# Kernel optimization log

Hardware: AMD Instinct MI355X
Metric: run time of the kernel (lower is better)

## Reference

```python
import jax, jax.numpy as jnp
import numpy as np

B, S, HID = 2, 2048, 3584
H, KV, D = 16, 8, 256
RQ, RK, RV = 6, 2, 2
GRP = H // KV
EPS = 1e-6
SOFTCAP = 50.0
SCALE = 256.0 ** -0.5  # query_pre_attn_scalar ** -0.5
NEG = -2.3819763e38


def _rmsnorm(x, w):
    # Gemma RMSNorm: fp32 normalize, scale by (1 + weight)
    xf = x.astype(jnp.float32)
    n = xf * jax.lax.rsqrt(jnp.mean(xf * xf, axis=-1, keepdims=True) + EPS)
    return (n * (1.0 + w)).astype(x.dtype)


def _rope_factor(x, freqs_cis):
    # x: [B,S,R,D]; freqs_cis: [S, D/2, 2] = (cos, sin)
    h = D // 2
    cos = freqs_cis[None, :, None, :, 0]  # [1,S,1,D/2]
    sin = freqs_cis[None, :, None, :, 1]
    x1, x2 = x[..., :h], x[..., h:]
    return jnp.concatenate([x1 * cos - x2 * sin, x2 * cos + x1 * sin], axis=-1)


def setup_inputs() -> dict:
    key = jax.random.key(0)
    ks = jax.random.split(key, 10)
    hidden_states = jax.random.normal(ks[0], (B, S, HID), dtype=jnp.float32)
    # rotary tables
    pos = jnp.arange(S, dtype=jnp.float32)
    inv = 1.0 / (10000.0 ** (jnp.arange(0, D, 2, dtype=jnp.float32) / D))
    ang = pos[:, None] * inv[None, :]                     # [S, D/2]
    freqs_cis = jnp.stack([jnp.cos(ang), jnp.sin(ang)], axis=-1)  # [S,D/2,2]
    kv_write_indices = jnp.arange(S, dtype=jnp.int32)
    k_cache_A = jnp.zeros((B, S, KV, RK), jnp.float32)
    k_cache_B = jnp.zeros((B, S, RK, D), jnp.float32)
    v_cache_A = jnp.zeros((B, S, KV, RV), jnp.float32)
    v_cache_B = jnp.zeros((B, S, RV, D), jnp.float32)
    causal = jnp.tril(jnp.ones((S, S), bool))
    mask = jnp.where(causal, 0.0, NEG)[None, None].astype(jnp.float32)
    sd = 1.0 / np.sqrt(HID)
    W_A_q = jax.random.normal(ks[1], (HID, H * RQ), jnp.float32) * sd
    W_A_k = jax.random.normal(ks[2], (HID, KV * RK), jnp.float32) * sd
    W_A_v = jax.random.normal(ks[3], (HID, KV * RV), jnp.float32) * sd
    W_B_q = jax.random.normal(ks[4], (HID, RQ * D), jnp.float32) * sd
    W_B_k = jax.random.normal(ks[5], (HID, RK * D), jnp.float32) * sd
    W_B_v = jax.random.normal(ks[6], (HID, RV * D), jnp.float32) * sd
    o_proj_w = jax.random.normal(ks[7], (H * D, HID), jnp.float32) * (1.0 / np.sqrt(H * D))
    q_norm_w = jnp.zeros((D,), jnp.float32)
    k_norm_w = jnp.zeros((D,), jnp.float32)
    return dict(hidden_states=hidden_states, freqs_cis=freqs_cis,
                kv_write_indices=kv_write_indices,
                k_cache_A=k_cache_A, k_cache_B=k_cache_B,
                v_cache_A=v_cache_A, v_cache_B=v_cache_B, mask=mask,
                W_A_q=W_A_q, W_A_k=W_A_k, W_A_v=W_A_v,
                W_B_q=W_B_q, W_B_k=W_B_k, W_B_v=W_B_v,
                o_proj_w=o_proj_w, q_norm_w=q_norm_w, k_norm_w=k_norm_w)


def reference(hidden_states, freqs_cis, kv_write_indices,
              k_cache_A, k_cache_B, v_cache_A, v_cache_B, mask,
              W_A_q, W_A_k, W_A_v, W_B_q, W_B_k, W_B_v,
              o_proj_w, q_norm_w, k_norm_w):
    hs = hidden_states
    # rank-factor projections (many small GEMMs)
    A_q = (hs @ W_A_q).reshape(B, S, H, RQ)
    A_k = (hs @ W_A_k).reshape(B, S, KV, RK)
    A_v = (hs @ W_A_v).reshape(B, S, KV, RV)
    B_q = (hs @ W_B_q).reshape(B, S, RQ, D)
    B_k = (hs @ W_B_k).reshape(B, S, RK, D)
    B_v = (hs @ W_B_v).reshape(B, S, RV, D)
    # qk-norm on low-rank B factors
    B_q = _rmsnorm(B_q, q_norm_w)
    B_k = _rmsnorm(B_k, k_norm_w)
    # RoPE on factors
    B_q = _rope_factor(B_q, freqs_cis)
    B_k = _rope_factor(B_k, freqs_cis)
    # factored KV cache write (prefill: indices = arange(S))
    kA = k_cache_A.at[:, kv_write_indices].set(A_k)
    kB = k_cache_B.at[:, kv_write_indices].set(B_k)
    vA = v_cache_A.at[:, kv_write_indices].set(A_v)
    vB = v_cache_B.at[:, kv_write_indices].set(B_v)
    # reconstruct Q/K/V from rank-R tensor products, divided by rank
    Q = jnp.einsum('bshr,bsrd->bshd', A_q.astype(jnp.float32),
                   B_q.astype(jnp.float32)) / RQ          # [B,S,H,D]
    K = jnp.einsum('bskr,bsrd->bskd', kA, kB) / RK        # [B,S,KV,D]
    V = jnp.einsum('bskr,bsrd->bskd', vA, vB) / RV
    Q = Q.astype(hs.dtype)
    # GQA expand
    K = jnp.repeat(K, GRP, axis=2)
    V = jnp.repeat(V, GRP, axis=2)
    q = jnp.transpose(Q, (0, 2, 1, 3)) * SCALE            # [B,H,S,D]
    k = jnp.transpose(K, (0, 2, 1, 3))
    v = jnp.transpose(V, (0, 2, 1, 3))
    scores = jnp.einsum('bhqd,bhkd->bhqk', q, k).astype(jnp.float32)
    scores = SOFTCAP * jnp.tanh(scores / SOFTCAP)
    scores = scores + mask
    probs = jax.nn.softmax(scores, axis=-1).astype(q.dtype)
    out = jnp.einsum('bhqk,bhkd->bhqd', probs, v)         # [B,H,S,D]
    out = jnp.transpose(out, (0, 2, 1, 3)).reshape(B, S, H * D)
    return out @ o_proj_w
```

## Files before the change

kernel.cpp:

```cpp
#include <hip/hip_runtime.h>

#define B_    2
#define S_    2048
#define HID_  3584
#define H_    16
#define KV_   8
#define D_    256
#define RQ_   6
#define NPROJ 2688
#define HD_   4096
#define MTOK  4096
#define EPS_  1e-6f
#define NEG_  -2.3819763e38f
#define SCALE_ 0.0625f

typedef unsigned short u16;
typedef __attribute__((ext_vector_type(8))) short short8;
typedef __attribute__((ext_vector_type(4))) float f32x4;

__device__ __forceinline__ u16 f2bf(float f) {
  unsigned u = __float_as_uint(f);
  u += 0x7fffu + ((u >> 16) & 1u);
  return (u16)(u >> 16);
}

__device__ __forceinline__ void gl_lds16(const void* g, void* l) {
  __builtin_amdgcn_global_load_lds((__attribute__((address_space(1))) void*)g,
                                   (__attribute__((address_space(3))) void*)l, 16, 0, 0);
}

__global__ __launch_bounds__(256) void cvt_f32_bf16(const float* __restrict__ src,
                                                    u16* __restrict__ dst, int n) {
  int i = blockIdx.x * 256 + threadIdx.x;
  const int stride = gridDim.x * 256;
  const int n4 = n >> 2;
  for (; i < n4; i += stride) {
    float4 v = ((const float4*)src)[i];
    ushort4 o;
    o.x = f2bf(v.x); o.y = f2bf(v.y); o.z = f2bf(v.z); o.w = f2bf(v.w);
    ((ushort4*)dst)[i] = o;
  }
}

__global__ __launch_bounds__(256) void transpose_f32_bf16(const float* __restrict__ src,
                                                          u16* __restrict__ dst, int R, int C) {
  __shared__ float tile[32][33];
  const int tx = threadIdx.x & 31, ty = threadIdx.x >> 5;
  const int r0 = blockIdx.x << 5, c0 = blockIdx.y << 5;
#pragma unroll
  for (int j = 0; j < 4; ++j) {
    int r = r0 + ty + j * 8, c = c0 + tx;
    tile[ty + j * 8][tx] = (r < R && c < C) ? src[(size_t)r * C + c] : 0.f;
  }
  __syncthreads();
#pragma unroll
  for (int j = 0; j < 4; ++j) {
    int cc = c0 + ty + j * 8, rr = r0 + tx;
    if (cc < C && rr < R) dst[(size_t)cc * R + rr] = f2bf(tile[tx][ty + j * 8]);
  }
}

__global__ __launch_bounds__(256) void transpose_bf16_b(const u16* __restrict__ src,
                                                        u16* __restrict__ dst, int R, int C) {
  __shared__ u16 tile[32][34];
  const size_t plane = (size_t)R * C;
  const u16* s = src + (size_t)blockIdx.z * plane;
  u16* d = dst + (size_t)blockIdx.z * plane;
  const int tx = threadIdx.x & 31, ty = threadIdx.x >> 5;
  const int r0 = blockIdx.x << 5, c0 = blockIdx.y << 5;
#pragma unroll
  for (int j = 0; j < 4; ++j) {
    int r = r0 + ty + j * 8, c = c0 + tx;
    tile[ty + j * 8][tx] = (r < R && c < C) ? s[(size_t)r * C + c] : (u16)0;
  }
  __syncthreads();
#pragma unroll
  for (int j = 0; j < 4; ++j) {
    int cc = c0 + ty + j * 8, rr = r0 + tx;
    if (cc < C && rr < R) d[(size_t)cc * R + rr] = tile[tx][ty + j * 8];
  }
}

__global__ __launch_bounds__(512, 2)
void gemm256(const u16* __restrict__ A, const u16* __restrict__ Bm, float* __restrict__ C,
             int N, int lda, int ldb, int ldc, int NT) {
  __shared__ __align__(16) u16 lds[2][2][2][8192];
  const int t = threadIdx.x;
  const int lane = t & 63;
  const int lq = lane & 15, lg = lane >> 4;
  const int w = t >> 6;
  const int wm = w >> 2, wn = w & 3;
  const int bm0 = blockIdx.x * 256, bn0 = blockIdx.y * 256;

  const int rsub = lane >> 2;
  const int ksub = (((lane & 3) ^ ((lane >> 3) & 3)) << 3);
  const u16* pa0 = A + (size_t)(bm0 + w * 16 + rsub) * lda + ksub;
  const u16* pa1 = pa0 + (size_t)128 * lda;
  const u16* pb0 = Bm + (size_t)(bn0 + w * 16 + rsub) * ldb + ksub;
  const u16* pb1 = pb0 + (size_t)128 * ldb;

  const int rdo = lq * 32 + ((lg ^ ((lq >> 1) & 3)) << 3);
  const int bsub = (wn & 1) << 3;

  f32x4 zero = {0.f, 0.f, 0.f, 0.f};
  f32x4 acc[8][4];
#pragma unroll
  for (int m = 0; m < 8; ++m)
#pragma unroll
    for (int n = 0; n < 4; ++n) acc[m][n] = zero;

  gl_lds16(pa0,      &lds[0][0][0][(w * 2 + 0) * 512]);
  gl_lds16(pa1,      &lds[0][0][1][(w * 2 + 0) * 512]);
  gl_lds16(pb0,      &lds[0][1][0][(w * 2 + 0) * 512]);
  gl_lds16(pb1,      &lds[0][1][1][(w * 2 + 0) * 512]);
  gl_lds16(pa0 + 32, &lds[0][0][0][(w * 2 + 1) * 512]);
  gl_lds16(pa1 + 32, &lds[0][0][1][(w * 2 + 1) * 512]);
  gl_lds16(pb0 + 32, &lds[0][1][0][(w * 2 + 1) * 512]);
  gl_lds16(pb1 + 32, &lds[0][1][1][(w * 2 + 1) * 512]);

  int cur = 0;
  for (int T = 0; T < NT; ++T) {
    const bool pre = (T + 1) < NT;
    const size_t ko = (size_t)(T + 1) * 64;
    const u16* ab = &lds[cur][0][wm][0];
    const u16* bb = &lds[cur][1][wn >> 1][0];
    const int nb = cur ^ 1;

    asm volatile("s_waitcnt vmcnt(4)" ::: "memory");
    __builtin_amdgcn_s_barrier();
    __builtin_amdgcn_sched_barrier(0);
    short8 af[4], bf[4];
#pragma unroll
    for (int m = 0; m < 4; ++m) af[m] = *(const short8*)(ab + (m * 2 + 0) * 512 + rdo);
#pragma unroll
    for (int n = 0; n < 4; ++n) bf[n] = *(const short8*)(bb + (bsub + n * 2 + 0) * 512 + rdo);
    if (pre) {
      gl_lds16(pa0 + ko, &lds[nb][0][0][(w * 2 + 0) * 512]);
      gl_lds16(pa1 + ko, &lds[nb][0][1][(w * 2 + 0) * 512]);
    }
    __builtin_amdgcn_s_setprio(1);
#pragma unroll
    for (int m = 0; m < 4; ++m)
#pragma unroll
      for (int n = 0; n < 4; ++n)
        acc[m][n] = __builtin_amdgcn_mfma_f32_16x16x32_bf16(af[m], bf[n], acc[m][n], 0, 0, 0);
    __builtin_amdgcn_s_setprio(0);

    short8 ag[4];
#pragma unroll
    for (int m = 0; m < 4; ++m) ag[m] = *(const short8*)(ab + ((m + 4) * 2 + 0) * 512 + rdo);
    if (pre) {
      gl_lds16(pb0 + ko, &lds[nb][1][0][(w * 2 + 0) * 512]);
      gl_lds16(pb1 + ko, &lds[nb][1][1][(w * 2 + 0) * 512]);
    }
    __builtin_amdgcn_s_setprio(1);
#pragma unroll
    for (int m = 0; m < 4; ++m)
#pragma unroll
      for (int n = 0; n < 4; ++n)
        acc[m + 4][n] = __builtin_amdgcn_mfma_f32_16x16x32_bf16(ag[m], bf[n], acc[m + 4][n], 0, 0, 0);
    __builtin_amdgcn_s_setprio(0);

    if (pre) { asm volatile("s_waitcnt vmcnt(4)" ::: "memory"); }
    else     { asm volatile("s_waitcnt vmcnt(0)" ::: "memory"); }
    __builtin_amdgcn_s_barrier();
    __builtin_amdgcn_sched_barrier(0);
    short8 af2[4], bf2[4];
#pragma unroll
    for (int m = 0; m < 4; ++m) af2[m] = *(const short8*)(ab + (m * 2 + 1) * 512 + rdo);
#pragma unroll
    for (int n = 0; n < 4; ++n) bf2[n] = *(const short8*)(bb + (bsub + n * 2 + 1) * 512 + rdo);
    if (pre) {
      gl_lds16(pa0 + ko + 32, &lds[nb][0][0][(w * 2 + 1) * 512]);
      gl_lds16(pa1 + ko + 32, &lds[nb][0][1][(w * 2 + 1) * 512]);
    }
    __builtin_amdgcn_s_setprio(1);
#pragma unroll
    for (int m = 0; m < 4; ++m)
#pragma unroll
      for (int n = 0; n < 4; ++n)
        acc[m][n] = __builtin_amdgcn_mfma_f32_16x16x32_bf16(af2[m], bf2[n], acc[m][n], 0, 0, 0);
    __builtin_amdgcn_s_setprio(0);

    short8 ag2[4];
#pragma unroll
    for (int m = 0; m < 4; ++m) ag2[m] = *(const short8*)(ab + ((m + 4) * 2 + 1) * 512 + rdo);
    if (pre) {
      gl_lds16(pb0 + ko + 32, &lds[nb][1][0][(w * 2 + 1) * 512]);
      gl_lds16(pb1 + ko + 32, &lds[nb][1][1][(w * 2 + 1) * 512]);
    }
    __builtin_amdgcn_s_setprio(1);
#pragma unroll
    for (int m = 0; m < 4; ++m)
#pragma unroll
      for (int n = 0; n < 4; ++n)
        acc[m + 4][n] = __builtin_amdgcn_mfma_f32_16x16x32_bf16(ag2[m], bf2[n], acc[m + 4][n], 0, 0, 0);
    __builtin_amdgcn_s_setprio(0);

    cur ^= 1;
  }

#pragma unroll
  for (int m = 0; m < 8; ++m) {
    const int row = bm0 + wm * 128 + m * 16 + lg * 4;
#pragma unroll
    for (int n = 0; n < 4; ++n) {
      const int col = bn0 + wn * 64 + n * 16 + lq;
      if (col < N) {
        float* cp = C + (size_t)row * ldc + col;
        cp[0] = acc[m][n][0];
        cp[(size_t)ldc] = acc[m][n][1];
        cp[(size_t)2 * ldc] = acc[m][n][2];
        cp[(size_t)3 * ldc] = acc[m][n][3];
      }
    }
  }
}

__global__ __launch_bounds__(256)
void build_qkv(const float* __restrict__ P, const float* __restrict__ freqs,
               const float* __restrict__ qw, const float* __restrict__ kw,
               u16* __restrict__ Qg, u16* __restrict__ Kg, u16* __restrict__ Vg) {
  const int token = blockIdx.x;
  const int b = token >> 11, s = token & 2047;
  const int d = threadIdx.x;
  const float* row = P + (size_t)token * NPROJ;
  __shared__ float aL[128];
  __shared__ float rQ[6][256];
  __shared__ float rK[2][256];
  __shared__ float red[4][8];

  if (d < 128) aL[d] = row[d];
  float bq[6], bk[2], bv[2];
#pragma unroll
  for (int r = 0; r < 6; ++r) bq[r] = row[128 + r * 256 + d];
#pragma unroll
  for (int r = 0; r < 2; ++r) bk[r] = row[1664 + r * 256 + d];
#pragma unroll
  for (int r = 0; r < 2; ++r) bv[r] = row[2176 + r * 256 + d];

  float sq[8];
#pragma unroll
  for (int r = 0; r < 6; ++r) sq[r] = bq[r] * bq[r];
  sq[6] = bk[0] * bk[0];
  sq[7] = bk[1] * bk[1];
#pragma unroll
  for (int j = 0; j < 8; ++j) {
    sq[j] += __shfl_xor(sq[j], 32, 64);
    sq[j] += __shfl_xor(sq[j], 16, 64);
    sq[j] += __shfl_xor(sq[j], 8, 64);
    sq[j] += __shfl_xor(sq[j], 4, 64);
    sq[j] += __shfl_xor(sq[j], 2, 64);
    sq[j] += __shfl_xor(sq[j], 1, 64);
  }
  const int lane = d & 63, wv = d >> 6;
  if (lane == 0) {
#pragma unroll
    for (int j = 0; j < 8; ++j) red[wv][j] = sq[j];
  }
  __syncthreads();
  float inv[8];
#pragma unroll
  for (int j = 0; j < 8; ++j) {
    float ss = red[0][j] + red[1][j] + red[2][j] + red[3][j];
    inv[j] = rsqrtf(ss * (1.0f / 256.0f) + EPS_);
  }
  const float gq = 1.f + qw[d], gk = 1.f + kw[d];
#pragma unroll
  for (int r = 0; r < 6; ++r) rQ[r][d] = bq[r] * inv[r] * gq;
#pragma unroll
  for (int r = 0; r < 2; ++r) rK[r][d] = bk[r] * inv[6 + r] * gk;
  __syncthreads();

  const int dh = d & 127;
  const float co = freqs[(s * 128 + dh) * 2 + 0];
  const float sn = freqs[(s * 128 + dh) * 2 + 1];
  float q_ro[6], k_ro[2];
  if (d < 128) {
#pragma unroll
    for (int r = 0; r < 6; ++r) q_ro[r] = rQ[r][d] * co - rQ[r][d + 128] * sn;
#pragma unroll
    for (int r = 0; r < 2; ++r) k_ro[r] = rK[r][d] * co - rK[r][d + 128] * sn;
  } else {
#pragma unroll
    for (int r = 0; r < 6; ++r) q_ro[r] = rQ[r][d] * co + rQ[r][d - 128] * sn;
#pragma unroll
    for (int r = 0; r < 2; ++r) k_ro[r] = rK[r][d] * co + rK[r][d - 128] * sn;
  }
  const float qs = SCALE_ * (1.0f / 6.0f);
#pragma unroll
  for (int h = 0; h < 16; ++h) {
    float a = 0.f;
#pragma unroll
    for (int r = 0; r < 6; ++r) a += aL[h * 6 + r] * q_ro[r];
    Qg[((size_t)(b * H_ + h) * S_ + s) * D_ + d] = f2bf(a * qs);
  }
#pragma unroll
  for (int kv = 0; kv < 8; ++kv) {
    float ak = aL[96 + kv * 2] * k_ro[0] + aL[96 + kv * 2 + 1] * k_ro[1];
    Kg[((size_t)(b * KV_ + kv) * S_ + s) * D_ + d] = f2bf(ak * 0.5f);
    float av = aL[112 + kv * 2] * bv[0] + aL[112 + kv * 2 + 1] * bv[1];
    Vg[((size_t)(b * KV_ + kv) * S_ + s) * D_ + d] = f2bf(av * 0.5f);
  }
}

__global__ __launch_bounds__(256, 2)
void attn_kernel(const u16* __restrict__ Qg, const u16* __restrict__ Kg,
                 const u16* __restrict__ VTg, u16* __restrict__ Og) {
  __shared__ __align__(16) u16 Kbuf[2][8192];
  __shared__ __align__(16) u16 Vbuf[2][8192];
  __shared__ __align__(16) u16 Pbuf[4][1024];

  const int t = threadIdx.x;
  const int lane = t & 63;
  const int lq = lane & 15, lg = lane >> 4;
  const int qw = t >> 6;
  const int h = blockIdx.x, b = blockIdx.y;
  const int qt = 15 - blockIdx.z;
  const int q0 = qt * 128;
  const int kvh = h >> 1;
  const int qbase = q0 + qw * 32;

  const u16* Kplane = Kg + (size_t)(b * KV_ + kvh) * S_ * D_;
  const u16* VTplane = VTg + (size_t)(b * KV_ + kvh) * D_ * S_;

  short8 qf[2][8];
#pragma unroll
  for (int qh = 0; qh < 2; ++qh) {
    const u16* Qrow = Qg + ((size_t)(b * H_ + h) * S_ + qbase + qh * 16 + lq) * D_;
#pragma unroll
    for (int ks = 0; ks < 8; ++ks) qf[qh][ks] = *(const short8*)(Qrow + ks * 32 + lg * 8);
  }

  int ksrc[4], vsrc[4];
#pragma unroll
  for (int i = 0; i < 4; ++i) {
    const int kr = i * 8 + (t >> 5);
    ksrc[i] = kr * D_ + (((t & 31) ^ (kr & 7)) << 3);
    const int vr = i * 64 + (t >> 2);
    vsrc[i] = vr * S_ + (((t & 3) ^ ((vr >> 1) & 3)) << 3);
  }

  f32x4 zero = {0.f, 0.f, 0.f, 0.f};
  f32x4 oacc[2][16];
#pragma unroll
  for (int qh = 0; qh < 2; ++qh)
#pragma unroll
    for (int db = 0; db < 16; ++db) oacc[qh][db] = zero;
  float m_s[2] = {NEG_, NEG_}, l_s[2] = {0.f, 0.f};

  const int nt = 4 * qt + 4;

#pragma unroll
  for (int i = 0; i < 4; ++i) {
    gl_lds16(Kplane + ksrc[i], &Kbuf[0][0] + (i * 256 + t) * 8);
    gl_lds16(VTplane + vsrc[i], &Vbuf[0][0] + (i * 256 + t) * 8);
  }
  __syncthreads();
  int cur = 0;
  for (int it = 0; it < nt; ++it) {
    const int kv0 = it * 32;
    if (it + 1 < nt) {
      const u16* kp = Kplane + (size_t)(it + 1) * 32 * D_;
      const u16* vp = VTplane + (it + 1) * 32;
      u16* kd = &Kbuf[cur ^ 1][0];
      u16* vd = &Vbuf[cur ^ 1][0];
#pragma unroll
      for (int i = 0; i < 4; ++i) {
        gl_lds16(kp + ksrc[i], kd + (i * 256 + t) * 8);
        gl_lds16(vp + vsrc[i], vd + (i * 256 + t) * 8);
      }
    }
    if (kv0 <= qbase + 31) {
      const u16* Kb = &Kbuf[cur][0];
      f32x4 sacc[2][2];
      sacc[0][0] = zero; sacc[0][1] = zero; sacc[1][0] = zero; sacc[1][1] = zero;
      __builtin_amdgcn_s_setprio(1);
#pragma unroll
      for (int kb = 0; kb < 2; ++kb) {
        const int rbase = (kb * 16 + lq) * 256;
        const int sw = lq & 7;
#pragma unroll
        for (int ks = 0; ks < 8; ++ks) {
          short8 kf = *(const short8*)(Kb + rbase + (((ks * 4 + lg) ^ sw) << 3));
          sacc[0][kb] = __builtin_amdgcn_mfma_f32_16x16x32_bf16(kf, qf[0][ks], sacc[0][kb], 0, 0, 0);
          sacc[1][kb] = __builtin_amdgcn_mfma_f32_16x16x32_bf16(kf, qf[1][ks], sacc[1][kb], 0, 0, 0);
        }
      }
      __builtin_amdgcn_s_setprio(0);
      float vmax[2];
#pragma unroll
      for (int qh = 0; qh < 2; ++qh) {
        const int qg = qbase + qh * 16 + lq;
        const bool tail = (kv0 + 31 > qbase + qh * 16);
        float vm = NEG_;
#pragma unroll
        for (int kb = 0; kb < 2; ++kb)
#pragma unroll
          for (int r = 0; r < 4; ++r) {
            float x = sacc[qh][kb][r];
            const float e = __expf(-fabsf(x) * 0.04f);
            const float th = (1.f - e) * __builtin_amdgcn_rcpf(1.f + e);
            x = copysignf(50.0f * th, x);
            if (tail && (kv0 + kb * 16 + lg * 4 + r > qg)) x = NEG_;
            sacc[qh][kb][r] = x;
            vm = fmaxf(vm, x);
          }
        vm = fmaxf(vm, __shfl_xor(vm, 16, 64));
        vm = fmaxf(vm, __shfl_xor(vm, 32, 64));
        vmax[qh] = vm;
      }
      const bool grow = (vmax[0] > m_s[0] + 8.f) | (vmax[1] > m_s[1] + 8.f);
      if (__any(grow)) {
        float c4[2][4];
#pragma unroll
        for (int qh = 0; qh < 2; ++qh) {
          const float mn = fmaxf(m_s[qh], vmax[qh]);
          const float c = __expf(m_s[qh] - mn);
          m_s[qh] = mn;
          l_s[qh] *= c;
#pragma unroll
          for (int r = 0; r < 4; ++r) c4[qh][r] = __shfl(c, lg * 4 + r, 16);
        }
#pragma unroll
        for (int qh = 0; qh < 2; ++qh)
#pragma unroll
          for (int db = 0; db < 16; ++db) {
            oacc[qh][db][0] *= c4[qh][0]; oacc[qh][db][1] *= c4[qh][1];
            oacc[qh][db][2] *= c4[qh][2]; oacc[qh][db][3] *= c4[qh][3];
          }
      }
#pragma unroll
      for (int qh = 0; qh < 2; ++qh) {
        float ps = 0.f;
#pragma unroll
        for (int kb = 0; kb < 2; ++kb)
#pragma unroll
          for (int r = 0; r < 4; ++r) {
            const float p = __expf(sacc[qh][kb][r] - m_s[qh]);
            sacc[qh][kb][r] = p;
            ps += p;
          }
        ps += __shfl_xor(ps, 16, 64);
        ps += __shfl_xor(ps, 32, 64);
        l_s[qh] += ps;
      }
      u16* Pw = &Pbuf[qw][0];
#pragma unroll
      for (int qh = 0; qh < 2; ++qh)
#pragma unroll
        for (int kb = 0; kb < 2; ++kb) {
          ushort4 pk;
          pk.x = f2bf(sacc[qh][kb][0]); pk.y = f2bf(sacc[qh][kb][1]);
          pk.z = f2bf(sacc[qh][kb][2]); pk.w = f2bf(sacc[qh][kb][3]);
          *(ushort4*)(Pw + qh * 512 + 8 * lq + 128 * (2 * kb + (lg >> 1)) + 4 * (lg & 1)) = pk;
        }
      short8 pf0 = *(const short8*)(Pw + lane * 8);
      short8 pf1 = *(const short8*)(Pw + 512 + lane * 8);
      const u16* Vb = &Vbuf[cur][0];
      __builtin_amdgcn_s_setprio(1);
#pragma unroll
      for (int db = 0; db < 16; ++db) {
        const int d = db * 16 + lq;
        short8 vf = *(const short8*)(Vb + d * 32 + ((lg ^ ((lq >> 1) & 3)) << 3));
        oacc[0][db] = __builtin_amdgcn_mfma_f32_16x16x32_bf16(pf0, vf, oacc[0][db], 0, 0, 0);
        oacc[1][db] = __builtin_amdgcn_mfma_f32_16x16x32_bf16(pf1, vf, oacc[1][db], 0, 0, 0);
      }
      __builtin_amdgcn_s_setprio(0);
    }
    __syncthreads();
    cur ^= 1;
  }
#pragma unroll
  for (int qh = 0; qh < 2; ++qh) {
    const float invl = __builtin_amdgcn_rcpf(l_s[qh]);
    float inv4[4];
#pragma unroll
    for (int r = 0; r < 4; ++r) inv4[r] = __shfl(invl, lg * 4 + r, 16);
#pragma unroll
    for (int r = 0; r < 4; ++r) {
      u16* orow = Og + (size_t)(b * S_ + qbase + qh * 16 + lg * 4 + r) * HD_ + h * D_;
#pragma unroll
      for (int db = 0; db < 16; ++db) orow[db * 16 + lq] = f2bf(oacc[qh][db][r] * inv4[r]);
    }
  }
}

extern "C" void kernel_launch(void* const* d_in, const int* in_sizes, int n_in,
                              void* d_out, int out_size, void* d_ws, size_t ws_size,
                              hipStream_t stream) {
  const float* hs    = (const float*)d_in[0];
  const float* freqs = (const float*)d_in[1];
  const float* W_A_q = (const float*)d_in[8];
  const float* W_A_k = (const float*)d_in[9];
  const float* W_A_v = (const float*)d_in[10];
  const float* W_B_q = (const float*)d_in[11];
  const float* W_B_k = (const float*)d_in[12];
  const float* W_B_v = (const float*)d_in[13];
  const float* Wo    = (const float*)d_in[14];
  const float* qw    = (const float*)d_in[15];
  const float* kw    = (const float*)d_in[16];
  float* out = (float*)d_out;

  char* ws = (char*)d_ws;
  u16* hsb = (u16*)(ws);
  u16* WT  = (u16*)(ws + 29360128);
  u16* WoT = (u16*)(ws + 48627712);
  u16* Qg  = (u16*)(ws + 77987840);
  u16* Kg  = (u16*)(ws + 111542272);
  u16* Vg  = (u16*)(ws + 128319488);
  u16* VTg = (u16*)(ws + 145096704);
  u16* AOg = (u16*)(ws + 161873920);
  float* Pout = (float*)d_out;

  cvt_f32_bf16<<<1024, 256, 0, stream>>>(hs, hsb, MTOK * HID_);
  transpose_f32_bf16<<<dim3(112, 3),   256, 0, stream>>>(W_A_q, WT + (size_t)0 * HID_,    HID_, 96);
  transpose_f32_bf16<<<dim3(112, 1),   256, 0, stream>>>(W_A_k, WT + (size_t)96 * HID_,   HID_, 16);
  transpose_f32_bf16<<<dim3(112, 1),   256, 0, stream>>>(W_A_v, WT + (size_t)112 * HID_,  HID_, 16);
  transpose_f32_bf16<<<dim3(112, 48),  256, 0, stream>>>(W_B_q, WT + (size_t)128 * HID_,  HID_, 1536);
  transpose_f32_bf16<<<dim3(112, 16),  256, 0, stream>>>(W_B_k, WT + (size_t)1664 * HID_, HID_, 512);
  transpose_f32_bf16<<<dim3(112, 16),  256, 0, stream>>>(W_B_v, WT + (size_t)2176 * HID_, HID_, 512);
  transpose_f32_bf16<<<dim3(128, 112), 256, 0, stream>>>(Wo, WoT, HD_, HID_);

  gemm256<<<dim3(16, 11), 512, 0, stream>>>(hsb, WT, Pout, NPROJ, HID_, HID_, NPROJ, 56);
  build_qkv<<<4096, 256, 0, stream>>>(Pout, freqs, qw, kw, Qg, Kg, Vg);
  transpose_bf16_b<<<dim3(64, 8, 16), 256, 0, stream>>>(Vg, VTg, S_, D_);
  attn_kernel<<<dim3(16, 2, 16), 256, 0, stream>>>(Qg, Kg, VTg, AOg);
  gemm256<<<dim3(16, 14), 512, 0, stream>>>(AOg, WoT, out, HID_, HD_, HD_, HID_, 64);
}
```

Baseline: 477.3 us.

## Software-pipeline GEMM LDS fragment loads across half-steps and interleave attention tile order

The GEMM main loop is restructured so each half-tile's LDS fragments (A, B and the second A group) are all loaded up front. The MFMAs for the previous half-step then run while those loads and the global prefetches are in flight, with a prologue wait and an epilogue drain added around the loop. The attention kernel's causal query-tile ordering changes from strictly descending to alternating long and short tiles, to balance work across concurrently resident blocks. This adds register pressure from holding two fragment sets, and changes barrier placement in a way that must stay race-free with the double-buffered LDS.

```diff
diff --git a/kernel.cpp b/kernel.cpp
--- a/kernel.cpp
+++ b/kernel.cpp
@@ -117,6 +117,11 @@
   gl_lds16(pa1 + 32, &lds[0][0][1][(w * 2 + 1) * 512]);
   gl_lds16(pb0 + 32, &lds[0][1][0][(w * 2 + 1) * 512]);
   gl_lds16(pb1 + 32, &lds[0][1][1][(w * 2 + 1) * 512]);
+  asm volatile("s_waitcnt vmcnt(4)" ::: "memory");
+  __builtin_amdgcn_s_barrier();
+
+  short8 a0[4], b0[4], g0[4];
+  short8 a1[4], b1[4], g1[4];
 
   int cur = 0;
   for (int T = 0; T < NT; ++T) {
@@ -126,66 +131,44 @@
     const u16* bb = &lds[cur][1][wn >> 1][0];
     const int nb = cur ^ 1;
 
-    asm volatile("s_waitcnt vmcnt(4)" ::: "memory");
-    __builtin_amdgcn_s_barrier();
-    __builtin_amdgcn_sched_barrier(0);
-    short8 af[4], bf[4];
-#pragma unroll
-    for (int m = 0; m < 4; ++m) af[m] = *(const short8*)(ab + (m * 2 + 0) * 512 + rdo);
-#pragma unroll
-    for (int n = 0; n < 4; ++n) bf[n] = *(const short8*)(bb + (bsub + n * 2 + 0) * 512 + rdo);
+#pragma unroll
+    for (int m = 0; m < 4; ++m) a0[m] = *(const short8*)(ab + (m * 2 + 0) * 512 + rdo);
+#pragma unroll
+    for (int n = 0; n < 4; ++n) b0[n] = *(const short8*)(bb + (bsub + n * 2 + 0) * 512 + rdo);
+#pragma unroll
+    for (int m = 0; m < 4; ++m) g0[m] = *(const short8*)(ab + ((m + 4) * 2 + 0) * 512 + rdo);
     if (pre) {
       gl_lds16(pa0 + ko, &lds[nb][0][0][(w * 2 + 0) * 512]);
       gl_lds16(pa1 + ko, &lds[nb][0][1][(w * 2 + 0) * 512]);
-    }
-    __builtin_amdgcn_s_setprio(1);
-#pragma unroll
-    for (int m = 0; m < 4; ++m)
-#pragma unroll
-      for (int n = 0; n < 4; ++n)
-        acc[m][n] = __builtin_amdgcn_mfma_f32_16x16x32_bf16(af[m], bf[n], acc[m][n], 0, 0, 0);
-    __builtin_amdgcn_s_setprio(0);
-
-    short8 ag[4];
-#pragma unroll
-    for (int m = 0; m < 4; ++m) ag[m] = *(const short8*)(ab + ((m + 4) * 2 + 0) * 512 + rdo);
-    if (pre) {
       gl_lds16(pb0 + ko, &lds[nb][1][0][(w * 2 + 0) * 512]);
       gl_lds16(pb1 + ko, &lds[nb][1][1][(w * 2 + 0) * 512]);
     }
-    __builtin_amdgcn_s_setprio(1);
-#pragma unroll
-    for (int m = 0; m < 4; ++m)
-#pragma unroll
-      for (int n = 0; n < 4; ++n)
-        acc[m + 4][n] = __builtin_amdgcn_mfma_f32_16x16x32_bf16(ag[m], bf[n], acc[m + 4][n], 0, 0, 0);
-    __builtin_amdgcn_s_setprio(0);
-
-    if (pre) { asm volatile("s_waitcnt vmcnt(4)" ::: "memory"); }
-    else     { asm volatile("s_waitcnt vmcnt(0)" ::: "memory"); }
+    if (T > 0) {
+      __builtin_amdgcn_s_setprio(1);
+#pragma unroll
+      for (int m = 0; m < 4; ++m)
+#pragma unroll
+        for (int n = 0; n < 4; ++n)
+          acc[m][n] = __builtin_amdgcn_mfma_f32_16x16x32_bf16(a1[m], b1[n], acc[m][n], 0, 0, 0);
+#pragma unroll
+      for (int m = 0; m < 4; ++m)
+#pragma unroll
+        for (int n = 0; n < 4; ++n)
+          acc[m + 4][n] = __builtin_amdgcn_mfma_f32_16x16x32_bf16(g1[m], b1[n], acc[m + 4][n], 0, 0, 0);
+      __builtin_amdgcn_s_setprio(0);
+    }
+    if (pre) { asm volatile("s_waitcnt vmcnt(4) lgkmcnt(0)" ::: "memory"); }
+    else     { asm volatile("s_waitcnt vmcnt(0) lgkmcnt(0)" ::: "memory"); }
     __builtin_amdgcn_s_barrier();
-    __builtin_amdgcn_sched_barrier(0);
-    short8 af2[4], bf2[4];
-#pragma unroll
-    for (int m = 0; m < 4; ++m) af2[m] = *(const short8*)(ab + (m * 2 + 1) * 512 + rdo);
-#pragma unroll
-    for (int n = 0; n < 4; ++n) bf2[n] = *(const short8*)(bb + (bsub + n * 2 + 1) * 512 + rdo);
+#pragma unroll
+    for (int m = 0; m < 4; ++m) a1[m] = *(const short8*)(ab + (m * 2 + 1) * 512 + rdo);
+#pragma unroll
+    for (int n = 0; n < 4; ++n) b1[n] = *(const short8*)(bb + (bsub + n * 2 + 1) * 512 + rdo);
+#pragma unroll
+    for (int m = 0; m < 4; ++m) g1[m] = *(const short8*)(ab + ((m + 4) * 2 + 1) * 512 + rdo);
     if (pre) {
       gl_lds16(pa0 + ko + 32, &lds[nb][0][0][(w * 2 + 1) * 512]);
       gl_lds16(pa1 + ko + 32, &lds[nb][0][1][(w * 2 + 1) * 512]);
-    }
-    __builtin_amdgcn_s_setprio(1);
-#pragma unroll
-    for (int m = 0; m < 4; ++m)
-#pragma unroll
-      for (int n = 0; n < 4; ++n)
-        acc[m][n] = __builtin_amdgcn_mfma_f32_16x16x32_bf16(af2[m], bf2[n], acc[m][n], 0, 0, 0);
-    __builtin_amdgcn_s_setprio(0);
-
-    short8 ag2[4];
-#pragma unroll
-    for (int m = 0; m < 4; ++m) ag2[m] = *(const short8*)(ab + ((m + 4) * 2 + 1) * 512 + rdo);
-    if (pre) {
       gl_lds16(pb0 + ko + 32, &lds[nb][1][0][(w * 2 + 1) * 512]);
       gl_lds16(pb1 + ko + 32, &lds[nb][1][1][(w * 2 + 1) * 512]);
     }
@@ -194,11 +177,31 @@
     for (int m = 0; m < 4; ++m)
 #pragma unroll
       for (int n = 0; n < 4; ++n)
-        acc[m + 4][n] = __builtin_amdgcn_mfma_f32_16x16x32_bf16(ag2[m], bf2[n], acc[m + 4][n], 0, 0, 0);
+        acc[m][n] = __builtin_amdgcn_mfma_f32_16x16x32_bf16(a0[m], b0[n], acc[m][n], 0, 0, 0);
+#pragma unroll
+    for (int m = 0; m < 4; ++m)
+#pragma unroll
+      for (int n = 0; n < 4; ++n)
+        acc[m + 4][n] = __builtin_amdgcn_mfma_f32_16x16x32_bf16(g0[m], b0[n], acc[m + 4][n], 0, 0, 0);
     __builtin_amdgcn_s_setprio(0);
-
+    if (pre) {
+      asm volatile("s_waitcnt vmcnt(4) lgkmcnt(0)" ::: "memory");
+      __builtin_amdgcn_s_barrier();
+    }
     cur ^= 1;
   }
+  __builtin_amdgcn_s_setprio(1);
+#pragma unroll
+  for (int m = 0; m < 4; ++m)
+#pragma unroll
+    for (int n = 0; n < 4; ++n)
+      acc[m][n] = __builtin_amdgcn_mfma_f32_16x16x32_bf16(a1[m], b1[n], acc[m][n], 0, 0, 0);
+#pragma unroll
+  for (int m = 0; m < 4; ++m)
+#pragma unroll
+    for (int n = 0; n < 4; ++n)
+      acc[m + 4][n] = __builtin_amdgcn_mfma_f32_16x16x32_bf16(g1[m], b1[n], acc[m + 4][n], 0, 0, 0);
+  __builtin_amdgcn_s_setprio(0);
 
 #pragma unroll
   for (int m = 0; m < 8; ++m) {
@@ -316,7 +319,8 @@
   const int lq = lane & 15, lg = lane >> 4;
   const int qw = t >> 6;
   const int h = blockIdx.x, b = blockIdx.y;
-  const int qt = 15 - blockIdx.z;
+  const int z = blockIdx.z;
+  const int qt = (z < 8) ? (15 - 2 * z) : (2 * z - 16);
   const int q0 = qt * 128;
   const int kvh = h >> 1;
   const int qbase = q0 + qw * 32;
```

Measured after the change: 485.8 us. About the same (+1.8%).
